# Kernel tuning notes

Measured on AMD Instinct MI355X. Metric: run time of the kernel, lower is better.

The kernel has to match this reference:

```python
import jax, jax.numpy as jnp
import numpy as np

N_NODES = 50000
N_EDGES = 800000
IN_CH = 128
HID = 128
NUM_CLASSES = 10
NUM_GRAPHS = 64


def _linear_params(key, fan_in, fan_out):
    kw, kb = jax.random.split(key)
    s = 1.0 / np.sqrt(fan_in)
    W = jax.random.uniform(kw, (fan_in, fan_out), jnp.float32, -s, s)
    b = jax.random.uniform(kb, (fan_out,), jnp.float32, -s, s)
    return W, b


def setup_inputs() -> dict:
    key = jax.random.key(0)
    ks = jax.random.split(key, 16)
    x = jax.random.normal(ks[0], (N_NODES, IN_CH), jnp.float32)
    edge_index = jax.random.randint(ks[1], (2, N_EDGES), 0, N_NODES, jnp.int64)
    batch = jnp.sort(jax.random.randint(ks[2], (N_NODES,), 0, NUM_GRAPHS, jnp.int64))
    inp = {"x": x, "edge_index": edge_index, "batch": batch}
    # conv layer 1 (in -> hid)
    inp["Wk1"], inp["bk1"] = _linear_params(ks[3], IN_CH, HID)
    inp["Wq1"], inp["bq1"] = _linear_params(ks[4], IN_CH, HID)
    inp["Wv1"], inp["bv1"] = _linear_params(ks[5], IN_CH, HID)
    inp["Ws1"], inp["bs1"] = _linear_params(ks[6], IN_CH, HID)
    inp["b1"] = jnp.zeros((HID,), jnp.float32)
    # conv layer 2 (hid -> hid)
    inp["Wk2"], inp["bk2"] = _linear_params(ks[7], HID, HID)
    inp["Wq2"], inp["bq2"] = _linear_params(ks[8], HID, HID)
    inp["Wv2"], inp["bv2"] = _linear_params(ks[9], HID, HID)
    inp["Ws2"], inp["bs2"] = _linear_params(ks[10], HID, HID)
    inp["b2"] = jnp.zeros((HID,), jnp.float32)
    # final fc
    inp["fcW"], inp["fcb"] = _linear_params(ks[11], HID, NUM_CLASSES)
    return inp


def _res_gated_conv(x, src, dst, Wk, bk, Wq, bq, Wv, bv, Ws, bs, b):
    # k from target node i, q and v from source node j (PyG ResGatedGraphConv)
    k = x @ Wk + bk            # [N, H]
    q = x @ Wq + bq            # [N, H]
    v = x @ Wv + bv            # [N, H]
    gate = jax.nn.sigmoid(k[dst] + q[src])   # [E, H]
    msg = gate * v[src]                       # [E, H]
    agg = jax.ops.segment_sum(msg, dst, num_segments=x.shape[0])
    return agg + x @ Ws + bs + b


def _global_mean_pool(x, batch, num_graphs):
    sums = jax.ops.segment_sum(x, batch, num_segments=num_graphs)
    cnts = jax.ops.segment_sum(jnp.ones((x.shape[0],), x.dtype), batch, num_segments=num_graphs)
    return sums / jnp.maximum(cnts, 1.0)[:, None]


def reference(x, edge_index, batch,
              Wk1, bk1, Wq1, bq1, Wv1, bv1, Ws1, bs1, b1,
              Wk2, bk2, Wq2, bq2, Wv2, bv2, Ws2, bs2, b2,
              fcW, fcb):
    src, dst = edge_index[0], edge_index[1]
    h = _res_gated_conv(x, src, dst, Wk1, bk1, Wq1, bq1, Wv1, bv1, Ws1, bs1, b1)
    h = jax.nn.relu(h)
    h = _res_gated_conv(h, src, dst, Wk2, bk2, Wq2, bq2, Wv2, bv2, Ws2, bs2, b2)
    h = jax.nn.relu(h)
    g = _global_mean_pool(h, batch, NUM_GRAPHS)   # [NUM_GRAPHS, HID]
    return g @ fcW + fcb                           # [NUM_GRAPHS, NUM_CLASSES]
```

## Files before the change

kernel.cpp:

```cpp
#include <hip/hip_runtime.h>
#include <math.h>


typedef __attribute__((ext_vector_type(8))) short short8;
typedef __attribute__((ext_vector_type(4))) float floatx4;
typedef __attribute__((ext_vector_type(8))) float floatx8;
typedef __attribute__((ext_vector_type(8))) unsigned short ushort8v;

#define LOG2E 1.4426950408889634f

__device__ __forceinline__ unsigned short f2b(float f) {
  unsigned int u = __builtin_bit_cast(unsigned int, f);
  u += 0x7fff + ((u >> 16) & 1);
  return (unsigned short)(u >> 16);
}
__device__ __forceinline__ float b2f(unsigned short u) {
  return __builtin_bit_cast(float, ((unsigned int)u) << 16);
}


__global__ __launch_bounds__(256) void hist_kernel(const int* __restrict__ dst,
                                                   int* __restrict__ cnt, int E) {
  int e = blockIdx.x * 256 + threadIdx.x;
  if (e < E) atomicAdd(&cnt[dst[e]], 1);
}

__global__ __launch_bounds__(256) void scan1_kernel(const int* __restrict__ cnt,
                                                    int* __restrict__ tmp_excl,
                                                    int* __restrict__ bsum, int n) {
  __shared__ int s[256];
  int t = threadIdx.x;
  int base = blockIdx.x * 512;
  int i0 = base + 2 * t, i1 = i0 + 1;
  int a0 = (i0 < n) ? cnt[i0] : 0;
  int a1 = (i1 < n) ? cnt[i1] : 0;
  int sum = a0 + a1;
  s[t] = sum;
  __syncthreads();
  for (int off = 1; off < 256; off <<= 1) {
    int v = (t >= off) ? s[t - off] : 0;
    __syncthreads();
    s[t] += v;
    __syncthreads();
  }
  int excl = s[t] - sum;
  if (i0 < n) tmp_excl[i0] = excl;
  if (i1 < n) tmp_excl[i1] = excl + a0;
  if (t == 255) bsum[blockIdx.x] = s[255];
}

__global__ __launch_bounds__(128) void scan2_kernel(const int* __restrict__ bsum,
                                                    int* __restrict__ boff, int nb) {
  __shared__ int s[128];
  int t = threadIdx.x;
  int v = (t < nb) ? bsum[t] : 0;
  s[t] = v;
  __syncthreads();
  for (int off = 1; off < 128; off <<= 1) {
    int u = (t >= off) ? s[t - off] : 0;
    __syncthreads();
    s[t] += u;
    __syncthreads();
  }
  if (t < nb) boff[t] = s[t] - v;
}

__global__ __launch_bounds__(256) void finalize_rp_kernel(const int* __restrict__ tmp_excl,
                                                          const int* __restrict__ boff,
                                                          int* __restrict__ row_ptr,
                                                          int* __restrict__ cursor,
                                                          int n, int E) {
  int i = blockIdx.x * 256 + threadIdx.x;
  if (i < n) {
    int v = tmp_excl[i] + boff[i >> 9];
    row_ptr[i] = v;
    cursor[i] = v;
  }
  if (i == 0) row_ptr[n] = E;
}

__global__ __launch_bounds__(256) void scatter_kernel(const int* __restrict__ src,
                                                      const int* __restrict__ dst,
                                                      int* __restrict__ cursor,
                                                      int* __restrict__ es, int E) {
  int e = blockIdx.x * 256 + threadIdx.x;
  if (e < E) {
    int i = dst[e];
    int p = atomicAdd(&cursor[i], 1);
    es[p] = src[e];
  }
}


__global__ __launch_bounds__(256) void prep_kernel(
    const float* __restrict__ X, unsigned short* __restrict__ Xb, int total4,
    const float* __restrict__ Wk1, const float* __restrict__ Wq1,
    const float* __restrict__ Wv1, const float* __restrict__ Ws1,
    const float* __restrict__ Wk2, const float* __restrict__ Wq2,
    const float* __restrict__ Wv2, const float* __restrict__ Ws2,
    unsigned short* __restrict__ WT,
    const float* __restrict__ bk1, const float* __restrict__ bq1,
    const float* __restrict__ bv1, const float* __restrict__ bs1,
    const float* __restrict__ b1,
    const float* __restrict__ bk2, const float* __restrict__ bq2,
    const float* __restrict__ bv2, const float* __restrict__ bs2,
    const float* __restrict__ b2,
    float* __restrict__ bcat, int nconvb) {
  int b = blockIdx.x;
  if (b < nconvb) {
    int i = b * 256 + threadIdx.x;
    if (i < total4) {
      float4 v = ((const float4*)X)[i];
      ushort4 o;
      o.x = f2b(v.x); o.y = f2b(v.y); o.z = f2b(v.z); o.w = f2b(v.w);
      ((ushort4*)Xb)[i] = o;
    }
    return;
  }
  b -= nconvb;
  if (b < 512) {
    int idx = b * 256 + threadIdx.x;
    int layer = idx >> 16;
    int rem = idx & 0xFFFF;
    int mat = rem >> 14;
    int nk = rem & 0x3FFF;
    int nn = nk >> 7, kk = nk & 127;
    int sel = layer * 4 + mat;
    const float* W = (sel == 0) ? Wk1 : (sel == 1) ? Wq1 : (sel == 2) ? Wv1 :
                     (sel == 3) ? Ws1 : (sel == 4) ? Wk2 : (sel == 5) ? Wq2 :
                     (sel == 6) ? Wv2 : Ws2;
    WT[idx] = f2b(W[kk * 128 + nn]);
    return;
  }
  b -= 512;
  {
    int idx = b * 256 + threadIdx.x;
    if (idx >= 1024) return;
    int layer = idx >> 9;
    int rem = idx & 511;
    int mat = rem >> 7, c = rem & 127;
    int sel = layer * 4 + mat;
    const float* bb = (sel == 0) ? bk1 : (sel == 1) ? bq1 : (sel == 2) ? bv1 :
                      (sel == 3) ? bs1 : (sel == 4) ? bk2 : (sel == 5) ? bq2 :
                      (sel == 6) ? bv2 : bs2;
    float v = bb[c];
    if (mat == 3) v += (layer == 0) ? b1[c] : b2[c];
    bcat[idx] = v;
  }
}


__global__ __launch_bounds__(256) void gemm_mfma_kernel(
    const unsigned short* __restrict__ Xb,
    const unsigned short* __restrict__ WT,
    const float* __restrict__ bcat,
    unsigned short* __restrict__ Kb, unsigned short* __restrict__ Qb,
    unsigned short* __restrict__ Vb, float* __restrict__ S, int n) {
  __shared__ unsigned short aT[128 * 136];

  int t = threadIdx.x;
  int row0 = blockIdx.x * 128;
  int m = blockIdx.y;

#pragma unroll
  for (int i = 0; i < 8; ++i) {
    int c = i * 256 + t;
    int r = c >> 4, col16 = c & 15;
    int4 v = make_int4(0, 0, 0, 0);
    if (row0 + r < n) v = *(const int4*)&Xb[(size_t)(row0 + r) * 128 + col16 * 8];
    *(int4*)&aT[r * 136 + col16 * 8] = v;
  }
  __syncthreads();

  int lane = t & 63, wid = t >> 6;
  int wy = wid >> 1, wx = wid & 1;
  int l15 = lane & 15, lq = lane >> 4;

  const unsigned short* WTm = WT + (size_t)m * 16384;

  floatx4 acc[4][4];
#pragma unroll
  for (int mf = 0; mf < 4; ++mf)
#pragma unroll
    for (int nf = 0; nf < 4; ++nf) acc[mf][nf] = (floatx4)(0.0f);

#pragma unroll
  for (int ks = 0; ks < 4; ++ks) {
    int kof = ks * 32 + lq * 8;
    short8 a[4], b[4];
#pragma unroll
    for (int mf = 0; mf < 4; ++mf)
      a[mf] = *(const short8*)&aT[(wy * 64 + mf * 16 + l15) * 136 + kof];
#pragma unroll
    for (int nf = 0; nf < 4; ++nf)
      b[nf] = *(const short8*)&WTm[(size_t)(wx * 64 + nf * 16 + l15) * 128 + kof];
#pragma unroll
    for (int mf = 0; mf < 4; ++mf)
#pragma unroll
      for (int nf = 0; nf < 4; ++nf)
        acc[mf][nf] = __builtin_amdgcn_mfma_f32_16x16x32_bf16(a[mf], b[nf], acc[mf][nf], 0, 0, 0);
  }

  __syncthreads();
  float* estage = (float*)aT + (size_t)wid * 1088;

  const float* bias = bcat + m * 128;
  int r4 = lane >> 2, cq4 = lane & 3;
  int col = wx * 64 + cq4 * 16;
  float4 bv[4];
#pragma unroll
  for (int j = 0; j < 4; ++j) bv[j] = *(const float4*)&bias[col + j * 4];

  unsigned short* Ob = (m == 0) ? Kb : (m == 1) ? Qb : Vb;

#pragma unroll
  for (int mf = 0; mf < 4; ++mf) {
#pragma unroll
    for (int nf = 0; nf < 4; ++nf)
#pragma unroll
      for (int i = 0; i < 4; ++i)
        estage[(lq * 4 + i) * 68 + nf * 16 + l15] = acc[mf][nf][i];
    int grow = row0 + wy * 64 + mf * 16 + r4;
    if (grow < n) {
      float4 p[4];
#pragma unroll
      for (int j = 0; j < 4; ++j) {
        float4 e = *(const float4*)&estage[r4 * 68 + cq4 * 16 + j * 4];
        p[j].x = e.x + bv[j].x; p[j].y = e.y + bv[j].y;
        p[j].z = e.z + bv[j].z; p[j].w = e.w + bv[j].w;
      }
      if (m < 3) {
        ushort8v o0, o1;
        o0[0] = f2b(p[0].x); o0[1] = f2b(p[0].y); o0[2] = f2b(p[0].z); o0[3] = f2b(p[0].w);
        o0[4] = f2b(p[1].x); o0[5] = f2b(p[1].y); o0[6] = f2b(p[1].z); o0[7] = f2b(p[1].w);
        o1[0] = f2b(p[2].x); o1[1] = f2b(p[2].y); o1[2] = f2b(p[2].z); o1[3] = f2b(p[2].w);
        o1[4] = f2b(p[3].x); o1[5] = f2b(p[3].y); o1[6] = f2b(p[3].z); o1[7] = f2b(p[3].w);
        *(ushort8v*)&Ob[(size_t)grow * 128 + col] = o0;
        *(ushort8v*)&Ob[(size_t)grow * 128 + col + 8] = o1;
      } else {
#pragma unroll
        for (int j = 0; j < 4; ++j)
          *(float4*)&S[(size_t)grow * 128 + col + j * 4] = p[j];
      }
    }
  }
}


__global__ __launch_bounds__(256) void edge_agg_kernel(
    const unsigned short* __restrict__ Kb, const unsigned short* __restrict__ Qb,
    const unsigned short* __restrict__ Vb, const float* __restrict__ S,
    const int* __restrict__ row_ptr, const int* __restrict__ es,
    unsigned short* __restrict__ Hb, float* __restrict__ Hf, int mode, int n) {
  int wid = threadIdx.x >> 6;
  int lane = threadIdx.x & 63;
  int node = blockIdx.x * 4 + wid;
  if (node >= n) return;
  int grp = lane >> 4;
  int l16 = lane & 15;

  ushort8v kr = *(const ushort8v*)&Kb[(size_t)node * 128 + l16 * 8];
  float kcn[8];
#pragma unroll
  for (int i = 0; i < 8; ++i) kcn[i] = b2f(kr[i]) * (-LOG2E);

  floatx8 acc = (floatx8)(0.0f);

  int e0 = row_ptr[node], e1 = row_ptr[node + 1];
  int e = e0 + grp;
  int j = (e < e1) ? es[e] : -1;
  while (j >= 0) {
    int en = e + 4;
    int jn = (en < e1) ? es[en] : -1;
    ushort8v q8 = *(const ushort8v*)&Qb[(size_t)j * 128 + l16 * 8];
    ushort8v v8 = *(const ushort8v*)&Vb[(size_t)j * 128 + l16 * 8];
#pragma unroll
    for (int i = 0; i < 8; ++i) {
      float q = b2f(q8[i]);
      float v = b2f(v8[i]);
      float ex = __builtin_amdgcn_exp2f(fmaf(q, -LOG2E, kcn[i]));
      acc[i] = fmaf(v, __builtin_amdgcn_rcpf(1.0f + ex), acc[i]);
    }
    e = en; j = jn;
  }

#pragma unroll
  for (int i = 0; i < 8; ++i) {
    acc[i] += __shfl_xor(acc[i], 16);
    acc[i] += __shfl_xor(acc[i], 32);
  }

  if (grp == 0) {
    float4 s0 = *(const float4*)&S[(size_t)node * 128 + l16 * 8];
    float4 s1 = *(const float4*)&S[(size_t)node * 128 + l16 * 8 + 4];
    float r[8];
    r[0] = fmaxf(acc[0] + s0.x, 0.f); r[1] = fmaxf(acc[1] + s0.y, 0.f);
    r[2] = fmaxf(acc[2] + s0.z, 0.f); r[3] = fmaxf(acc[3] + s0.w, 0.f);
    r[4] = fmaxf(acc[4] + s1.x, 0.f); r[5] = fmaxf(acc[5] + s1.y, 0.f);
    r[6] = fmaxf(acc[6] + s1.z, 0.f); r[7] = fmaxf(acc[7] + s1.w, 0.f);
    if (mode == 0) {
      ushort8v o;
#pragma unroll
      for (int i = 0; i < 8; ++i) o[i] = f2b(r[i]);
      *(ushort8v*)&Hb[(size_t)node * 128 + l16 * 8] = o;
    } else {
      float4 h0 = make_float4(r[0], r[1], r[2], r[3]);
      float4 h1 = make_float4(r[4], r[5], r[6], r[7]);
      *(float4*)&Hf[(size_t)node * 128 + l16 * 8] = h0;
      *(float4*)&Hf[(size_t)node * 128 + l16 * 8 + 4] = h1;
    }
  }
}


__device__ __forceinline__ int lb_batch(const int* __restrict__ batch, int n, int key) {
  int lo = 0, hi = n;
  while (lo < hi) {
    int mid = (lo + hi) >> 1;
    if (batch[mid] < key) lo = mid + 1; else hi = mid;
  }
  return lo;
}

__global__ __launch_bounds__(256) void pool_sum_kernel(const float* __restrict__ Hf,
                                                       const int* __restrict__ batch,
                                                       float* __restrict__ pool, int n) {
  __shared__ float red[8 * 128];
  int g = blockIdx.x >> 4;
  int slice = blockIdx.x & 15;
  int t = threadIdx.x;
  int grp = t >> 5;
  int cq = t & 31;
  int s = lb_batch(batch, n, g), e = lb_batch(batch, n, g + 1);
  int cnt = e - s;
  int per = (cnt + 15) >> 4;
  int ss = s + slice * per;
  int ee = ss + per; if (ee > e) ee = e;

  float4 acc = make_float4(0.f, 0.f, 0.f, 0.f);
  const float4* H4 = (const float4*)Hf;
  for (int nd = ss + grp; nd < ee; nd += 8) {
    float4 v = H4[(size_t)nd * 32 + cq];
    acc.x += v.x; acc.y += v.y; acc.z += v.z; acc.w += v.w;
  }
  *(float4*)&red[grp * 128 + cq * 4] = acc;
  __syncthreads();
  if (t < 128) {
    float tot = 0.f;
#pragma unroll
    for (int g8 = 0; g8 < 8; ++g8) tot += red[g8 * 128 + t];
    if (tot != 0.f) atomicAdd(&pool[g * 128 + t], tot);
  }
}

__global__ __launch_bounds__(128) void fc_kernel(const float* __restrict__ pool,
                                                 const int* __restrict__ batch,
                                                 const float* __restrict__ fcW,
                                                 const float* __restrict__ fcb,
                                                 float* __restrict__ out, int n) {
  __shared__ float p[128];
  int g = blockIdx.x;
  int t = threadIdx.x;
  int cnt = lb_batch(batch, n, g + 1) - lb_batch(batch, n, g);
  float inv = 1.0f / (float)((cnt > 0) ? cnt : 1);
  p[t] = pool[g * 128 + t] * inv;
  __syncthreads();
  if (t < 10) {
    float s = fcb[t];
    for (int c = 0; c < 128; ++c) s += p[c] * fcW[c * 10 + t];
    out[g * 10 + t] = s;
  }
}


extern "C" void kernel_launch(void* const* d_in, const int* in_sizes, int n_in,
                              void* d_out, int out_size, void* d_ws, size_t ws_size,
                              hipStream_t stream) {
  const float* x   = (const float*)d_in[0];
  const int* eidx  = (const int*)d_in[1];
  const int* batch = (const int*)d_in[2];
  const float* Wk1 = (const float*)d_in[3];  const float* bk1 = (const float*)d_in[4];
  const float* Wq1 = (const float*)d_in[5];  const float* bq1 = (const float*)d_in[6];
  const float* Wv1 = (const float*)d_in[7];  const float* bv1 = (const float*)d_in[8];
  const float* Ws1 = (const float*)d_in[9];  const float* bs1 = (const float*)d_in[10];
  const float* b1  = (const float*)d_in[11];
  const float* Wk2 = (const float*)d_in[12]; const float* bk2 = (const float*)d_in[13];
  const float* Wq2 = (const float*)d_in[14]; const float* bq2 = (const float*)d_in[15];
  const float* Wv2 = (const float*)d_in[16]; const float* bv2 = (const float*)d_in[17];
  const float* Ws2 = (const float*)d_in[18]; const float* bs2 = (const float*)d_in[19];
  const float* b2  = (const float*)d_in[20];
  const float* fcW = (const float*)d_in[21]; const float* fcb = (const float*)d_in[22];
  float* out = (float*)d_out;

  const int N = in_sizes[0] / 128;
  const int E = in_sizes[1] / 2;
  const int* src = eidx;
  const int* dst = eidx + E;

  char* w = (char*)d_ws;
  size_t off = 0;
  auto carve = [&](size_t bytes) -> void* {
    void* p = w + off;
    off += (bytes + 255) & ~size_t(255);
    return p;
  };
  const size_t featB16 = (size_t)N * 128 * 2;
  const size_t featB32 = (size_t)N * 128 * 4;
  unsigned short* Xb = (unsigned short*)carve(featB16);
  unsigned short* Kb = (unsigned short*)carve(featB16);
  unsigned short* Qb = (unsigned short*)carve(featB16);
  unsigned short* Vb = (unsigned short*)carve(featB16);
  unsigned short* Hb = (unsigned short*)carve(featB16);
  float* S  = (float*)carve(featB32);
  float* Hf = (float*)carve(featB32);
  unsigned short* WT = (unsigned short*)carve(2 * 4 * 128 * 128 * 2);
  float* bcat = (float*)carve(1024 * 4);
  int* cnt      = (int*)carve((size_t)N * 4);
  int* row_ptr  = (int*)carve((size_t)(N + 1) * 4);
  int* cursor   = (int*)carve((size_t)N * 4);
  int* tmp_excl = (int*)carve((size_t)N * 4);
  int* bsum     = (int*)carve(256 * 4);
  int* boff     = (int*)carve(256 * 4);
  int* es       = (int*)carve((size_t)E * 4);
  float* pool   = (float*)carve(64 * 128 * 4);
  (void)ws_size; (void)n_in; (void)out_size;

  hipMemsetAsync(cnt, 0, (size_t)N * 4, stream);
  hipMemsetAsync(pool, 0, 64 * 128 * 4, stream);

  int nb512 = (N + 511) / 512;
  hist_kernel<<<(E + 255) / 256, 256, 0, stream>>>(dst, cnt, E);
  scan1_kernel<<<nb512, 256, 0, stream>>>(cnt, tmp_excl, bsum, N);
  scan2_kernel<<<1, 128, 0, stream>>>(bsum, boff, nb512);
  finalize_rp_kernel<<<(N + 255) / 256, 256, 0, stream>>>(tmp_excl, boff, row_ptr, cursor, N, E);
  scatter_kernel<<<(E + 255) / 256, 256, 0, stream>>>(src, dst, cursor, es, E);

  int nconvb = (N * 32 + 255) / 256;
  prep_kernel<<<nconvb + 512 + 4, 256, 0, stream>>>(
      x, Xb, N * 32,
      Wk1, Wq1, Wv1, Ws1, Wk2, Wq2, Wv2, Ws2, WT,
      bk1, bq1, bv1, bs1, b1, bk2, bq2, bv2, bs2, b2, bcat, nconvb);

  dim3 ggrid((N + 127) / 128, 4);

  gemm_mfma_kernel<<<ggrid, 256, 0, stream>>>(Xb, WT, bcat, Kb, Qb, Vb, S, N);
  edge_agg_kernel<<<(N + 3) / 4, 256, 0, stream>>>(Kb, Qb, Vb, S, row_ptr, es,
                                                   Hb, Hf, 0, N);

  gemm_mfma_kernel<<<ggrid, 256, 0, stream>>>(Hb, WT + 65536, bcat + 512,
                                              Kb, Qb, Vb, S, N);
  edge_agg_kernel<<<(N + 3) / 4, 256, 0, stream>>>(Kb, Qb, Vb, S, row_ptr, es,
                                                   Hb, Hf, 1, N);

  pool_sum_kernel<<<1024, 256, 0, stream>>>(Hf, batch, pool, N);
  fc_kernel<<<64, 128, 0, stream>>>(pool, batch, fcW, fcb, out, N);
}
```

Measured before the change: 427.6 us.

## Trim launches, widen edge gather to 8 edges per wave, pool from bf16

Folds the scan2 pass into finalize_rp by redoing the block-offset scan in each block. The two memsets are replaced by zeroing cnt inside prep_kernel, and pool atomics become per-slice partials summed in fc_kernel. The edge aggregation kernel now walks 8 edges per wave with 16 channels per lane, using wider loads and bf16 unpack helpers. The second layer's output stays bf16, so the fp32 Hf buffer is dropped and the pool reads less memory, at the cost of some precision in the pooled sum.

```diff
diff --git a/kernel.cpp b/kernel.cpp
--- a/kernel.cpp
+++ b/kernel.cpp
@@ -4,7 +4,6 @@
 
 typedef __attribute__((ext_vector_type(8))) short short8;
 typedef __attribute__((ext_vector_type(4))) float floatx4;
-typedef __attribute__((ext_vector_type(8))) float floatx8;
 typedef __attribute__((ext_vector_type(8))) unsigned short ushort8v;
 
 #define LOG2E 1.4426950408889634f
@@ -16,6 +15,12 @@
 }
 __device__ __forceinline__ float b2f(unsigned short u) {
   return __builtin_bit_cast(float, ((unsigned int)u) << 16);
+}
+__device__ __forceinline__ float blo(unsigned int u) {
+  return __builtin_bit_cast(float, u << 16);
+}
+__device__ __forceinline__ float bhi(unsigned int u) {
+  return __builtin_bit_cast(float, u & 0xffff0000u);
 }
 
 
@@ -49,30 +54,26 @@
   if (t == 255) bsum[blockIdx.x] = s[255];
 }
 
-__global__ __launch_bounds__(128) void scan2_kernel(const int* __restrict__ bsum,
-                                                    int* __restrict__ boff, int nb) {
+__global__ __launch_bounds__(256) void finalize_rp_kernel(const int* __restrict__ tmp_excl,
+                                                          const int* __restrict__ bsum,
+                                                          int* __restrict__ row_ptr,
+                                                          int* __restrict__ cursor,
+                                                          int n, int E, int nb) {
   __shared__ int s[128];
   int t = threadIdx.x;
-  int v = (t < nb) ? bsum[t] : 0;
-  s[t] = v;
+  if (t < 128) s[t] = (t < nb) ? bsum[t] : 0;
   __syncthreads();
   for (int off = 1; off < 128; off <<= 1) {
-    int u = (t >= off) ? s[t - off] : 0;
+    int v = (t < 128 && t >= off) ? s[t - off] : 0;
     __syncthreads();
-    s[t] += u;
+    if (t < 128) s[t] += v;
     __syncthreads();
   }
-  if (t < nb) boff[t] = s[t] - v;
-}
-
-__global__ __launch_bounds__(256) void finalize_rp_kernel(const int* __restrict__ tmp_excl,
-                                                          const int* __restrict__ boff,
-                                                          int* __restrict__ row_ptr,
-                                                          int* __restrict__ cursor,
-                                                          int n, int E) {
-  int i = blockIdx.x * 256 + threadIdx.x;
+  int chunk = blockIdx.x >> 1;
+  int boff = (chunk == 0) ? 0 : s[chunk - 1];
+  int i = blockIdx.x * 256 + t;
   if (i < n) {
-    int v = tmp_excl[i] + boff[i >> 9];
+    int v = tmp_excl[i] + boff;
     row_ptr[i] = v;
     cursor[i] = v;
   }
@@ -105,7 +106,8 @@
     const float* __restrict__ bk2, const float* __restrict__ bq2,
     const float* __restrict__ bv2, const float* __restrict__ bs2,
     const float* __restrict__ b2,
-    float* __restrict__ bcat, int nconvb) {
+    float* __restrict__ bcat,
+    int* __restrict__ cnt, int ncnt4, int nconvb, int nzerob) {
   int b = blockIdx.x;
   if (b < nconvb) {
     int i = b * 256 + threadIdx.x;
@@ -118,6 +120,12 @@
     return;
   }
   b -= nconvb;
+  if (b < nzerob) {
+    int i = b * 256 + threadIdx.x;
+    if (i < ncnt4) ((int4*)cnt)[i] = make_int4(0, 0, 0, 0);
+    return;
+  }
+  b -= nzerob;
   if (b < 512) {
     int idx = b * 256 + threadIdx.x;
     int layer = idx >> 16;
@@ -251,64 +259,94 @@
     const unsigned short* __restrict__ Kb, const unsigned short* __restrict__ Qb,
     const unsigned short* __restrict__ Vb, const float* __restrict__ S,
     const int* __restrict__ row_ptr, const int* __restrict__ es,
-    unsigned short* __restrict__ Hb, float* __restrict__ Hf, int mode, int n) {
+    unsigned short* __restrict__ Hb, int n) {
   int wid = threadIdx.x >> 6;
   int lane = threadIdx.x & 63;
   int node = blockIdx.x * 4 + wid;
   if (node >= n) return;
-  int grp = lane >> 4;
-  int l16 = lane & 15;
-
-  ushort8v kr = *(const ushort8v*)&Kb[(size_t)node * 128 + l16 * 8];
-  float kcn[8];
-#pragma unroll
-  for (int i = 0; i < 8; ++i) kcn[i] = b2f(kr[i]) * (-LOG2E);
-
-  floatx8 acc = (floatx8)(0.0f);
+  int slot = lane >> 3;
+  int l8 = lane & 7;
+  int chb = l8 * 16;
+
+  uint4 k0 = *(const uint4*)&Kb[(size_t)node * 128 + chb];
+  uint4 k1 = *(const uint4*)&Kb[(size_t)node * 128 + chb + 8];
+  float kcn[16];
+#pragma unroll
+  for (int p = 0; p < 4; ++p) {
+    unsigned int u0 = ((const unsigned int*)&k0)[p];
+    unsigned int u1 = ((const unsigned int*)&k1)[p];
+    kcn[2 * p]     = blo(u0) * (-LOG2E);
+    kcn[2 * p + 1] = bhi(u0) * (-LOG2E);
+    kcn[8 + 2 * p]     = blo(u1) * (-LOG2E);
+    kcn[8 + 2 * p + 1] = bhi(u1) * (-LOG2E);
+  }
+
+  float acc[16];
+#pragma unroll
+  for (int i = 0; i < 16; ++i) acc[i] = 0.0f;
 
   int e0 = row_ptr[node], e1 = row_ptr[node + 1];
-  int e = e0 + grp;
+  int e = e0 + slot;
   int j = (e < e1) ? es[e] : -1;
   while (j >= 0) {
-    int en = e + 4;
+    int en = e + 8;
     int jn = (en < e1) ? es[en] : -1;
-    ushort8v q8 = *(const ushort8v*)&Qb[(size_t)j * 128 + l16 * 8];
-    ushort8v v8 = *(const ushort8v*)&Vb[(size_t)j * 128 + l16 * 8];
-#pragma unroll
-    for (int i = 0; i < 8; ++i) {
-      float q = b2f(q8[i]);
-      float v = b2f(v8[i]);
-      float ex = __builtin_amdgcn_exp2f(fmaf(q, -LOG2E, kcn[i]));
-      acc[i] = fmaf(v, __builtin_amdgcn_rcpf(1.0f + ex), acc[i]);
+    uint4 q0 = *(const uint4*)&Qb[(size_t)j * 128 + chb];
+    uint4 q1 = *(const uint4*)&Qb[(size_t)j * 128 + chb + 8];
+    uint4 v0 = *(const uint4*)&Vb[(size_t)j * 128 + chb];
+    uint4 v1 = *(const uint4*)&Vb[(size_t)j * 128 + chb + 8];
+#pragma unroll
+    for (int p = 0; p < 4; ++p) {
+      unsigned int qu0 = ((const unsigned int*)&q0)[p];
+      unsigned int qu1 = ((const unsigned int*)&q1)[p];
+      unsigned int vu0 = ((const unsigned int*)&v0)[p];
+      unsigned int vu1 = ((const unsigned int*)&v1)[p];
+      {
+        float ex = __builtin_amdgcn_exp2f(fmaf(blo(qu0), -LOG2E, kcn[2 * p]));
+        acc[2 * p] = fmaf(blo(vu0), __builtin_amdgcn_rcpf(1.0f + ex), acc[2 * p]);
+      }
+      {
+        float ex = __builtin_amdgcn_exp2f(fmaf(bhi(qu0), -LOG2E, kcn[2 * p + 1]));
+        acc[2 * p + 1] = fmaf(bhi(vu0), __builtin_amdgcn_rcpf(1.0f + ex), acc[2 * p + 1]);
+      }
+      {
+        float ex = __builtin_amdgcn_exp2f(fmaf(blo(qu1), -LOG2E, kcn[8 + 2 * p]));
+        acc[8 + 2 * p] = fmaf(blo(vu1), __builtin_amdgcn_rcpf(1.0f + ex), acc[8 + 2 * p]);
+      }
+      {
+        float ex = __builtin_amdgcn_exp2f(fmaf(bhi(qu1), -LOG2E, kcn[8 + 2 * p + 1]));
+        acc[8 + 2 * p + 1] = fmaf(bhi(vu1), __builtin_amdgcn_rcpf(1.0f + ex), acc[8 + 2 * p + 1]);
+      }
     }
     e = en; j = jn;
   }
 
 #pragma unroll
-  for (int i = 0; i < 8; ++i) {
+  for (int i = 0; i < 16; ++i) {
+    acc[i] += __shfl_xor(acc[i], 8);
     acc[i] += __shfl_xor(acc[i], 16);
     acc[i] += __shfl_xor(acc[i], 32);
   }
 
-  if (grp == 0) {
-    float4 s0 = *(const float4*)&S[(size_t)node * 128 + l16 * 8];
-    float4 s1 = *(const float4*)&S[(size_t)node * 128 + l16 * 8 + 4];
-    float r[8];
-    r[0] = fmaxf(acc[0] + s0.x, 0.f); r[1] = fmaxf(acc[1] + s0.y, 0.f);
-    r[2] = fmaxf(acc[2] + s0.z, 0.f); r[3] = fmaxf(acc[3] + s0.w, 0.f);
-    r[4] = fmaxf(acc[4] + s1.x, 0.f); r[5] = fmaxf(acc[5] + s1.y, 0.f);
-    r[6] = fmaxf(acc[6] + s1.z, 0.f); r[7] = fmaxf(acc[7] + s1.w, 0.f);
-    if (mode == 0) {
-      ushort8v o;
-#pragma unroll
-      for (int i = 0; i < 8; ++i) o[i] = f2b(r[i]);
-      *(ushort8v*)&Hb[(size_t)node * 128 + l16 * 8] = o;
-    } else {
-      float4 h0 = make_float4(r[0], r[1], r[2], r[3]);
-      float4 h1 = make_float4(r[4], r[5], r[6], r[7]);
-      *(float4*)&Hf[(size_t)node * 128 + l16 * 8] = h0;
-      *(float4*)&Hf[(size_t)node * 128 + l16 * 8 + 4] = h1;
+  if (slot == 0) {
+    ushort8v o0, o1;
+#pragma unroll
+    for (int q = 0; q < 4; ++q) {
+      float4 sv = *(const float4*)&S[(size_t)node * 128 + chb + q * 4];
+      float r0 = fmaxf(acc[q * 4 + 0] + sv.x, 0.f);
+      float r1 = fmaxf(acc[q * 4 + 1] + sv.y, 0.f);
+      float r2 = fmaxf(acc[q * 4 + 2] + sv.z, 0.f);
+      float r3 = fmaxf(acc[q * 4 + 3] + sv.w, 0.f);
+      if (q < 2) {
+        o0[q * 4 + 0] = f2b(r0); o0[q * 4 + 1] = f2b(r1);
+        o0[q * 4 + 2] = f2b(r2); o0[q * 4 + 3] = f2b(r3);
+      } else {
+        o1[(q - 2) * 4 + 0] = f2b(r0); o1[(q - 2) * 4 + 1] = f2b(r1);
+        o1[(q - 2) * 4 + 2] = f2b(r2); o1[(q - 2) * 4 + 3] = f2b(r3);
+      }
     }
+    *(ushort8v*)&Hb[(size_t)node * 128 + chb] = o0;
+    *(ushort8v*)&Hb[(size_t)node * 128 + chb + 8] = o1;
   }
 }
 
@@ -322,9 +360,9 @@
   return lo;
 }
 
-__global__ __launch_bounds__(256) void pool_sum_kernel(const float* __restrict__ Hf,
+__global__ __launch_bounds__(256) void pool_sum_kernel(const unsigned short* __restrict__ Hb,
                                                        const int* __restrict__ batch,
-                                                       float* __restrict__ pool, int n) {
+                                                       float* __restrict__ partial, int n) {
   __shared__ float red[8 * 128];
   int g = blockIdx.x >> 4;
   int slice = blockIdx.x & 15;
@@ -338,10 +376,10 @@
   int ee = ss + per; if (ee > e) ee = e;
 
   float4 acc = make_float4(0.f, 0.f, 0.f, 0.f);
-  const float4* H4 = (const float4*)Hf;
   for (int nd = ss + grp; nd < ee; nd += 8) {
-    float4 v = H4[(size_t)nd * 32 + cq];
-    acc.x += v.x; acc.y += v.y; acc.z += v.z; acc.w += v.w;
+    uint2 u = *(const uint2*)&Hb[(size_t)nd * 128 + cq * 4];
+    acc.x += blo(u.x); acc.y += bhi(u.x);
+    acc.z += blo(u.y); acc.w += bhi(u.y);
   }
   *(float4*)&red[grp * 128 + cq * 4] = acc;
   __syncthreads();
@@ -349,11 +387,11 @@
     float tot = 0.f;
 #pragma unroll
     for (int g8 = 0; g8 < 8; ++g8) tot += red[g8 * 128 + t];
-    if (tot != 0.f) atomicAdd(&pool[g * 128 + t], tot);
-  }
-}
-
-__global__ __launch_bounds__(128) void fc_kernel(const float* __restrict__ pool,
+    partial[(size_t)slice * 8192 + g * 128 + t] = tot;
+  }
+}
+
+__global__ __launch_bounds__(128) void fc_kernel(const float* __restrict__ partial,
                                                  const int* __restrict__ batch,
                                                  const float* __restrict__ fcW,
                                                  const float* __restrict__ fcb,
@@ -363,7 +401,10 @@
   int t = threadIdx.x;
   int cnt = lb_batch(batch, n, g + 1) - lb_batch(batch, n, g);
   float inv = 1.0f / (float)((cnt > 0) ? cnt : 1);
-  p[t] = pool[g * 128 + t] * inv;
+  float tot = 0.f;
+#pragma unroll
+  for (int s = 0; s < 16; ++s) tot += partial[(size_t)s * 8192 + g * 128 + t];
+  p[t] = tot * inv;
   __syncthreads();
   if (t < 10) {
     float s = fcb[t];
@@ -412,46 +453,42 @@
   unsigned short* Vb = (unsigned short*)carve(featB16);
   unsigned short* Hb = (unsigned short*)carve(featB16);
   float* S  = (float*)carve(featB32);
-  float* Hf = (float*)carve(featB32);
   unsigned short* WT = (unsigned short*)carve(2 * 4 * 128 * 128 * 2);
   float* bcat = (float*)carve(1024 * 4);
-  int* cnt      = (int*)carve((size_t)N * 4);
+  int* cnt      = (int*)carve(((size_t)N + 4) * 4);
   int* row_ptr  = (int*)carve((size_t)(N + 1) * 4);
   int* cursor   = (int*)carve((size_t)N * 4);
   int* tmp_excl = (int*)carve((size_t)N * 4);
   int* bsum     = (int*)carve(256 * 4);
-  int* boff     = (int*)carve(256 * 4);
   int* es       = (int*)carve((size_t)E * 4);
-  float* pool   = (float*)carve(64 * 128 * 4);
+  float* partial = (float*)carve((size_t)16 * 64 * 128 * 4);
   (void)ws_size; (void)n_in; (void)out_size;
 
-  hipMemsetAsync(cnt, 0, (size_t)N * 4, stream);
-  hipMemsetAsync(pool, 0, 64 * 128 * 4, stream);
+  int nconvb = (N * 32 + 255) / 256;
+  int ncnt4 = (N + 3) / 4;
+  int nzerob = (ncnt4 + 255) / 256;
+  prep_kernel<<<nconvb + nzerob + 512 + 4, 256, 0, stream>>>(
+      x, Xb, N * 32,
+      Wk1, Wq1, Wv1, Ws1, Wk2, Wq2, Wv2, Ws2, WT,
+      bk1, bq1, bv1, bs1, b1, bk2, bq2, bv2, bs2, b2, bcat,
+      cnt, ncnt4, nconvb, nzerob);
 
   int nb512 = (N + 511) / 512;
   hist_kernel<<<(E + 255) / 256, 256, 0, stream>>>(dst, cnt, E);
   scan1_kernel<<<nb512, 256, 0, stream>>>(cnt, tmp_excl, bsum, N);
-  scan2_kernel<<<1, 128, 0, stream>>>(bsum, boff, nb512);
-  finalize_rp_kernel<<<(N + 255) / 256, 256, 0, stream>>>(tmp_excl, boff, row_ptr, cursor, N, E);
+  finalize_rp_kernel<<<(N + 255) / 256, 256, 0, stream>>>(tmp_excl, bsum, row_ptr,
+                                                          cursor, N, E, nb512);
   scatter_kernel<<<(E + 255) / 256, 256, 0, stream>>>(src, dst, cursor, es, E);
 
-  int nconvb = (N * 32 + 255) / 256;
-  prep_kernel<<<nconvb + 512 + 4, 256, 0, stream>>>(
-      x, Xb, N * 32,
-      Wk1, Wq1, Wv1, Ws1, Wk2, Wq2, Wv2, Ws2, WT,
-      bk1, bq1, bv1, bs1, b1, bk2, bq2, bv2, bs2, b2, bcat, nconvb);
-
   dim3 ggrid((N + 127) / 128, 4);
 
   gemm_mfma_kernel<<<ggrid, 256, 0, stream>>>(Xb, WT, bcat, Kb, Qb, Vb, S, N);
-  edge_agg_kernel<<<(N + 3) / 4, 256, 0, stream>>>(Kb, Qb, Vb, S, row_ptr, es,
-                                                   Hb, Hf, 0, N);
+  edge_agg_kernel<<<(N + 3) / 4, 256, 0, stream>>>(Kb, Qb, Vb, S, row_ptr, es, Hb, N);
 
   gemm_mfma_kernel<<<ggrid, 256, 0, stream>>>(Hb, WT + 65536, bcat + 512,
                                               Kb, Qb, Vb, S, N);
-  edge_agg_kernel<<<(N + 3) / 4, 256, 0, stream>>>(Kb, Qb, Vb, S, row_ptr, es,
-                                                   Hb, Hf, 1, N);
-
-  pool_sum_kernel<<<1024, 256, 0, stream>>>(Hf, batch, pool, N);
-  fc_kernel<<<64, 128, 0, stream>>>(pool, batch, fcW, fcb, out, N);
-}
+  edge_agg_kernel<<<(N + 3) / 4, 256, 0, stream>>>(Kb, Qb, Vb, S, row_ptr, es, Hb, N);
+
+  pool_sum_kernel<<<1024, 256, 0, stream>>>(Hb, batch, partial, N);
+  fc_kernel<<<64, 128, 0, stream>>>(partial, batch, fcW, fcb, out, N);
+}
```

Result: no change. 423.8 us (-0.9%).
